# Optimization experiments

Hardware: AMD Instinct MI355X
Metric: run time of the kernel (lower is better)

## Reference

```python
import jax, jax.numpy as jnp
import numpy as np

B, S, D = 2, 2048, 768
HD = 64          # hardcoded head_dim in module
NH = D // HD     # 12 query heads
NKV = max(1, NH // 3)  # 4 kv heads
GROUPS = NH // NKV     # 3
WINDOW = 384
THETA = 10000.0
EPS = 1e-6


def setup_inputs() -> dict:
    key = jax.random.key(0)
    ks = jax.random.split(key, 5)
    return {
        "hidden_states": jax.random.normal(ks[0], (B, S, D), dtype=jnp.float32),
        "q_w": jax.random.normal(ks[1], (NH * HD, D), dtype=jnp.float32) * 0.02,
        "k_w": jax.random.normal(ks[2], (NKV * HD, D), dtype=jnp.float32) * 0.02,
        "v_w": jax.random.normal(ks[3], (NKV * HD, D), dtype=jnp.float32) * 0.02,
        "o_w": jax.random.normal(ks[4], (D, NH * HD), dtype=jnp.float32) * 0.02,
        "q_ln_w": jnp.ones((HD,), dtype=jnp.float32),
        "k_ln_w": jnp.ones((HD,), dtype=jnp.float32),
    }


def _rmsnorm(x, w):
    var = jnp.mean(jnp.square(x.astype(jnp.float32)), axis=-1, keepdims=True)
    return w * (x * jax.lax.rsqrt(var + EPS)).astype(x.dtype)


def _rotate_half(x):
    x1, x2 = jnp.split(x, 2, axis=-1)
    return jnp.concatenate((-x2, x1), axis=-1)


def _rope_cos_sin(seq_len, dtype):
    inv_freq = 1.0 / (THETA ** (jnp.arange(0, HD, 2, dtype=jnp.float32) / HD))
    t = jnp.arange(seq_len, dtype=jnp.float32)
    freqs = jnp.outer(t, inv_freq)            # [S, HD/2]
    emb = jnp.concatenate((freqs, freqs), -1)  # [S, HD]
    return jnp.cos(emb).astype(dtype), jnp.sin(emb).astype(dtype)


def reference(hidden_states, q_w, k_w, v_w, o_w, q_ln_w, k_ln_w):
    b, s, _ = hidden_states.shape
    # projections (nn.Linear: y = x @ W.T)
    q = hidden_states @ q_w.T   # [B,S,NH*HD]
    k = hidden_states @ k_w.T   # [B,S,NKV*HD]
    v = hidden_states @ v_w.T

    q = _rmsnorm(q.reshape(b, s, NH, HD), q_ln_w).transpose(0, 2, 1, 3)      # [B,NH,S,HD]
    k = _rmsnorm(k.reshape(b, s, NKV, HD), k_ln_w).transpose(0, 2, 1, 3)     # [B,NKV,S,HD]
    v = v.reshape(b, s, NKV, HD).transpose(0, 2, 1, 3)                       # [B,NKV,S,HD]

    cos, sin = _rope_cos_sin(s, q.dtype)  # [S,HD]
    cos = cos[None, None]
    sin = sin[None, None]
    q = q * cos + _rotate_half(q) * sin
    k = k * cos + _rotate_half(k) * sin

    # grouped-query repeat: [B,NKV,S,HD] -> [B,NH,S,HD]
    k = jnp.repeat(k, GROUPS, axis=1)
    v = jnp.repeat(v, GROUPS, axis=1)

    scores = jnp.einsum("bhqd,bhkd->bhqk", q, k) / np.sqrt(HD)
    # causal + sliding-window mask: allow i-WINDOW < j <= i
    idx = jnp.arange(s)
    rel = idx[None, :] - idx[:, None]  # j - i
    allowed = (rel <= 0) & (rel > -WINDOW)
    scores = jnp.where(allowed[None, None], scores, -jnp.inf)

    attn = jax.nn.softmax(scores.astype(jnp.float32), axis=-1).astype(q.dtype)
    out = jnp.einsum("bhqk,bhkd->bhqd", attn, v)       # [B,NH,S,HD]
    out = out.transpose(0, 2, 1, 3).reshape(b, s, NH * HD)
    return out @ o_w.T
```

## Files before the change

kernel.cpp:

```cpp
#include <hip/hip_runtime.h>
#include <hip/hip_bf16.h>

typedef __hip_bfloat16 bf16;
typedef __attribute__((ext_vector_type(8))) short bf16x8;
typedef __attribute__((ext_vector_type(4))) float f32x4;

#define MFMA16(a, b, c) __builtin_amdgcn_mfma_f32_16x16x32_bf16((a), (b), (c), 0, 0, 0)


__device__ __forceinline__ void st4bf(bf16* p, float4 v) {
    bf16 t[4];
    t[0] = __float2bfloat16(v.x); t[1] = __float2bfloat16(v.y);
    t[2] = __float2bfloat16(v.z); t[3] = __float2bfloat16(v.w);
    *reinterpret_cast<uint2*>(p) = *reinterpret_cast<const uint2*>(t);
}

__global__ __launch_bounds__(256) void k_prep(
    const float* __restrict__ hs, const float* __restrict__ qw,
    const float* __restrict__ kw, const float* __restrict__ vw,
    const float* __restrict__ ow,
    bf16* __restrict__ hsb, bf16* __restrict__ qwb, bf16* __restrict__ kwb,
    bf16* __restrict__ vwb, bf16* __restrict__ owb, float2* __restrict__ tab)
{
    const int bid = blockIdx.x, tid = threadIdx.x;
    const float* src; bf16* dst; int rel;
    if (bid < 3072)      { src = hs; dst = hsb; rel = bid; }
    else if (bid < 3648) { src = qw; dst = qwb; rel = bid - 3072; }
    else if (bid < 3840) { src = kw; dst = kwb; rel = bid - 3648; }
    else if (bid < 4032) { src = vw; dst = vwb; rel = bid - 3840; }
    else if (bid < 4608) { src = ow; dst = owb; rel = bid - 4032; }
    else {
        int i = (bid - 4608) * 256 + tid;
        int f = i & 31;
        float ang = (float)(i >> 5) * expf(-(float)f * 0.28782313662425572f);
        float sn, cs; sincosf(ang, &sn, &cs);
        tab[i] = make_float2(cs, sn);
        return;
    }
    int i = (rel * 256 + tid) * 4;
    float4 v = *reinterpret_cast<const float4*>(src + i);
    st4bf(dst + i, v);
}

__global__ __launch_bounds__(256) void k_qkv(
    const bf16* __restrict__ hsb, const bf16* __restrict__ qwb,
    const bf16* __restrict__ kwb, const bf16* __restrict__ vwb,
    const float* __restrict__ qln, const float* __restrict__ kln,
    const float2* __restrict__ tab,
    bf16* __restrict__ qo, bf16* __restrict__ ko, bf16* __restrict__ vto)
{
    __shared__ bf16 As[2][64 * 72];
    __shared__ bf16 Bs[2][64 * 72];
    const int tid = threadIdx.x;
    const int w = tid >> 6, l = tid & 63;
    const int lm = l & 15, lg = l >> 4;
    const int m0 = blockIdx.x * 64;
    const int nblk = blockIdx.y;

    const bf16* wsrc; int wrow0, kind, head;
    if (nblk < 12)      { wsrc = qwb; wrow0 = nblk * 64;        kind = 0; head = nblk; }
    else if (nblk < 16) { wsrc = kwb; wrow0 = (nblk - 12) * 64; kind = 1; head = nblk - 12; }
    else                { wsrc = vwb; wrow0 = (nblk - 16) * 64; kind = 2; head = nblk - 16; }

    const int sr = tid >> 2, sc = (tid & 3) * 16;
    const bf16* aptr = hsb  + (size_t)(m0 + sr) * 768 + sc;
    const bf16* bptr = wsrc + (size_t)(wrow0 + sr) * 768 + sc;

    bf16x8 ra0 = *(const bf16x8*)(aptr);
    bf16x8 ra1 = *(const bf16x8*)(aptr + 8);
    bf16x8 rb0 = *(const bf16x8*)(bptr);
    bf16x8 rb1 = *(const bf16x8*)(bptr + 8);
    *(bf16x8*)(&As[0][sr * 72 + sc])     = ra0;
    *(bf16x8*)(&As[0][sr * 72 + sc + 8]) = ra1;
    *(bf16x8*)(&Bs[0][sr * 72 + sc])     = rb0;
    *(bf16x8*)(&Bs[0][sr * 72 + sc + 8]) = rb1;
    __syncthreads();

    f32x4 acc[4] = {};
    for (int t = 0; t < 12; ++t) {
        const int p = t & 1;
        if (t < 11) {
            const bf16* ap = aptr + (t + 1) * 64;
            const bf16* bp = bptr + (t + 1) * 64;
            ra0 = *(const bf16x8*)(ap);
            ra1 = *(const bf16x8*)(ap + 8);
            rb0 = *(const bf16x8*)(bp);
            rb1 = *(const bf16x8*)(bp + 8);
        }
        #pragma unroll
        for (int kk = 0; kk < 2; ++kk) {
            bf16x8 af = *(const bf16x8*)(&As[p][(w * 16 + lm) * 72 + kk * 32 + lg * 8]);
            #pragma unroll
            for (int ct = 0; ct < 4; ++ct) {
                bf16x8 bfr = *(const bf16x8*)(&Bs[p][(ct * 16 + lm) * 72 + kk * 32 + lg * 8]);
                acc[ct] = MFMA16(af, bfr, acc[ct]);
            }
        }
        if (t < 11) {
            __syncthreads();
            *(bf16x8*)(&As[p ^ 1][sr * 72 + sc])     = ra0;
            *(bf16x8*)(&As[p ^ 1][sr * 72 + sc + 8]) = ra1;
            *(bf16x8*)(&Bs[p ^ 1][sr * 72 + sc])     = rb0;
            *(bf16x8*)(&Bs[p ^ 1][sr * 72 + sc + 8]) = rb1;
            __syncthreads();
        }
    }

    const int b  = m0 >> 11;
    const int s0 = m0 & 2047;

    if (kind == 2) {
        bf16* base = vto + (size_t)(b * 4 + head) * 64 * 2048;
        #pragma unroll
        for (int r = 0; r < 4; ++r) {
            const int s = s0 + w * 16 + lg * 4 + r;
            #pragma unroll
            for (int ct = 0; ct < 4; ++ct)
                base[(size_t)(ct * 16 + lm) * 2048 + s] = __float2bfloat16(acc[ct][r]);
        }
        return;
    }

    const float* ln = (kind == 0) ? qln : kln;
    float lw[4];
    #pragma unroll
    for (int ct = 0; ct < 4; ++ct) lw[ct] = ln[ct * 16 + lm];

    bf16* base = (kind == 0) ? qo + ((size_t)(b * 12 + head) * 2048 + s0) * 64
                             : ko + ((size_t)(b * 4  + head) * 2048 + s0) * 64;
    #pragma unroll
    for (int r = 0; r < 4; ++r) {
        float n0 = acc[0][r], n1 = acc[1][r], n2 = acc[2][r], n3 = acc[3][r];
        float ss = n0 * n0 + n1 * n1 + n2 * n2 + n3 * n3;
        ss += __shfl_xor(ss, 1);
        ss += __shfl_xor(ss, 2);
        ss += __shfl_xor(ss, 4);
        ss += __shfl_xor(ss, 8);
        float rms = rsqrtf(ss * (1.0f / 64.0f) + 1e-6f);
        n0 *= rms * lw[0]; n1 *= rms * lw[1]; n2 *= rms * lw[2]; n3 *= rms * lw[3];
        const int row = w * 16 + lg * 4 + r;
        const float2* tp = tab + (size_t)(s0 + row) * 32;
        float2 t0 = tp[lm], t1 = tp[lm + 16];
        bf16* dst = base + (size_t)row * 64;
        dst[lm]      = __float2bfloat16(n0 * t0.x - n2 * t0.y);
        dst[lm + 16] = __float2bfloat16(n1 * t1.x - n3 * t1.y);
        dst[lm + 32] = __float2bfloat16(n2 * t0.x + n0 * t0.y);
        dst[lm + 48] = __float2bfloat16(n3 * t1.x + n1 * t1.y);
    }
}

__global__ __launch_bounds__(256) void k_attn(
    const bf16* __restrict__ qi, const bf16* __restrict__ ki,
    const bf16* __restrict__ vti, bf16* __restrict__ ao)
{
    __shared__ bf16 Ks[2][64 * 72];
    __shared__ bf16 Vs[2][64 * 72];
    __shared__ bf16 Ps[64 * 72];
    const int tid = threadIdx.x;
    const int w = tid >> 6, l = tid & 63;
    const int lm = l & 15, lg = l >> 4;
    const int qb = blockIdx.x, h = blockIdx.y, b = blockIdx.z;
    const int kv = h / 3;
    const int q0 = qb * 64;

    const bf16* qbase = qi + ((size_t)((b * 12 + h) * 2048 + q0 + w * 16 + lm)) * 64 + lg * 8;
    bf16x8 qf0 = *(const bf16x8*)(qbase);
    bf16x8 qf1 = *(const bf16x8*)(qbase + 32);

    f32x4 oacc[4] = {};
    float m_[4], l_[4];
    #pragma unroll
    for (int r = 0; r < 4; ++r) { m_[r] = -INFINITY; l_[r] = 0.f; }

    const int sr = tid >> 2, sc = (tid & 3) * 16;
    const bf16* kgb = ki  + (size_t)(b * 4 + kv) * 2048 * 64;
    const bf16* vgb = vti + (size_t)(b * 4 + kv) * 64 * 2048;

    const int kb_lo = (qb > 6) ? (qb - 6) : 0;
    {
        const bf16* kp = kgb + (size_t)(kb_lo * 64 + sr) * 64 + sc;
        const bf16* vp = vgb + (size_t)sr * 2048 + kb_lo * 64 + sc;
        *(bf16x8*)(&Ks[0][sr * 72 + sc])     = *(const bf16x8*)(kp);
        *(bf16x8*)(&Ks[0][sr * 72 + sc + 8]) = *(const bf16x8*)(kp + 8);
        *(bf16x8*)(&Vs[0][sr * 72 + sc])     = *(const bf16x8*)(vp);
        *(bf16x8*)(&Vs[0][sr * 72 + sc + 8]) = *(const bf16x8*)(vp + 8);
    }
    __syncthreads();

    for (int kb = kb_lo; kb <= qb; ++kb) {
        const int p = (kb - kb_lo) & 1;
        const int k0 = kb * 64;

        bf16x8 rk0, rk1, rv0, rv1;
        if (kb < qb) {
            const bf16* kp = kgb + (size_t)(k0 + 64 + sr) * 64 + sc;
            const bf16* vp = vgb + (size_t)sr * 2048 + k0 + 64 + sc;
            rk0 = *(const bf16x8*)(kp);
            rk1 = *(const bf16x8*)(kp + 8);
            rv0 = *(const bf16x8*)(vp);
            rv1 = *(const bf16x8*)(vp + 8);
        }

        f32x4 sacc[4];
        #pragma unroll
        for (int kt = 0; kt < 4; ++kt) {
            bf16x8 kf0 = *(const bf16x8*)(&Ks[p][(kt * 16 + lm) * 72 + lg * 8]);
            bf16x8 kf1 = *(const bf16x8*)(&Ks[p][(kt * 16 + lm) * 72 + 32 + lg * 8]);
            f32x4 z = {0.f, 0.f, 0.f, 0.f};
            z = MFMA16(qf0, kf0, z);
            sacc[kt] = MFMA16(qf1, kf1, z);
        }

        float pmax[4] = {-INFINITY, -INFINITY, -INFINITY, -INFINITY};
        #pragma unroll
        for (int kt = 0; kt < 4; ++kt)
            #pragma unroll
            for (int r = 0; r < 4; ++r) {
                int kgl = k0 + kt * 16 + lm;
                int qgl = q0 + w * 16 + lg * 4 + r;
                bool ok = (kgl <= qgl) && (kgl > qgl - 384);
                float s = ok ? sacc[kt][r] * 0.125f : -INFINITY;
                sacc[kt][r] = s;
                pmax[r] = fmaxf(pmax[r], s);
            }
        #pragma unroll
        for (int r = 0; r < 4; ++r) {
            float t = pmax[r];
            t = fmaxf(t, __shfl_xor(t, 1));
            t = fmaxf(t, __shfl_xor(t, 2));
            t = fmaxf(t, __shfl_xor(t, 4));
            t = fmaxf(t, __shfl_xor(t, 8));
            pmax[r] = t;
        }

        #pragma unroll
        for (int r = 0; r < 4; ++r) {
            float mnew = fmaxf(m_[r], pmax[r]);
            float scale, rs = 0.f, pv[4];
            if (mnew > -INFINITY) {
                scale = expf(m_[r] - mnew);
                #pragma unroll
                for (int kt = 0; kt < 4; ++kt) { pv[kt] = expf(sacc[kt][r] - mnew); rs += pv[kt]; }
            } else {
                scale = 1.f;
                #pragma unroll
                for (int kt = 0; kt < 4; ++kt) pv[kt] = 0.f;
            }
            m_[r] = mnew;
            rs += __shfl_xor(rs, 1);
            rs += __shfl_xor(rs, 2);
            rs += __shfl_xor(rs, 4);
            rs += __shfl_xor(rs, 8);
            l_[r] = l_[r] * scale + rs;
            #pragma unroll
            for (int dt = 0; dt < 4; ++dt) oacc[dt][r] *= scale;
            #pragma unroll
            for (int kt = 0; kt < 4; ++kt)
                Ps[(w * 16 + lg * 4 + r) * 72 + kt * 16 + lm] = __float2bfloat16(pv[kt]);
        }

        bf16x8 pf0 = *(const bf16x8*)(&Ps[(w * 16 + lm) * 72 + lg * 8]);
        bf16x8 pf1 = *(const bf16x8*)(&Ps[(w * 16 + lm) * 72 + 32 + lg * 8]);
        #pragma unroll
        for (int dt = 0; dt < 4; ++dt) {
            bf16x8 vf0 = *(const bf16x8*)(&Vs[p][(dt * 16 + lm) * 72 + lg * 8]);
            bf16x8 vf1 = *(const bf16x8*)(&Vs[p][(dt * 16 + lm) * 72 + 32 + lg * 8]);
            oacc[dt] = MFMA16(pf0, vf0, oacc[dt]);
            oacc[dt] = MFMA16(pf1, vf1, oacc[dt]);
        }

        if (kb < qb) {
            __syncthreads();
            *(bf16x8*)(&Ks[p ^ 1][sr * 72 + sc])     = rk0;
            *(bf16x8*)(&Ks[p ^ 1][sr * 72 + sc + 8]) = rk1;
            *(bf16x8*)(&Vs[p ^ 1][sr * 72 + sc])     = rv0;
            *(bf16x8*)(&Vs[p ^ 1][sr * 72 + sc + 8]) = rv1;
            __syncthreads();
        }
    }

    #pragma unroll
    for (int r = 0; r < 4; ++r) {
        float inv = 1.f / l_[r];
        bf16* dst = ao + ((size_t)(b * 2048 + q0 + w * 16 + lg * 4 + r)) * 768 + h * 64;
        #pragma unroll
        for (int dt = 0; dt < 4; ++dt)
            dst[dt * 16 + lm] = __float2bfloat16(oacc[dt][r] * inv);
    }
}

__global__ __launch_bounds__(256) void k_oproj(
    const bf16* __restrict__ A, const bf16* __restrict__ W, float* __restrict__ out)
{
    __shared__ bf16 As[2][64 * 72];
    __shared__ bf16 Bs[2][64 * 72];
    const int tid = threadIdx.x;
    const int w = tid >> 6, l = tid & 63;
    const int lm = l & 15, lg = l >> 4;
    const int m0 = blockIdx.x * 64, n0 = blockIdx.y * 64;

    const int sr = tid >> 2, sc = (tid & 3) * 16;
    const bf16* aptr = A + (size_t)(m0 + sr) * 768 + sc;
    const bf16* bptr = W + (size_t)(n0 + sr) * 768 + sc;

    bf16x8 ra0 = *(const bf16x8*)(aptr);
    bf16x8 ra1 = *(const bf16x8*)(aptr + 8);
    bf16x8 rb0 = *(const bf16x8*)(bptr);
    bf16x8 rb1 = *(const bf16x8*)(bptr + 8);
    *(bf16x8*)(&As[0][sr * 72 + sc])     = ra0;
    *(bf16x8*)(&As[0][sr * 72 + sc + 8]) = ra1;
    *(bf16x8*)(&Bs[0][sr * 72 + sc])     = rb0;
    *(bf16x8*)(&Bs[0][sr * 72 + sc + 8]) = rb1;
    __syncthreads();

    f32x4 acc[4] = {};
    for (int t = 0; t < 12; ++t) {
        const int p = t & 1;
        if (t < 11) {
            const bf16* ap = aptr + (t + 1) * 64;
            const bf16* bp = bptr + (t + 1) * 64;
            ra0 = *(const bf16x8*)(ap);
            ra1 = *(const bf16x8*)(ap + 8);
            rb0 = *(const bf16x8*)(bp);
            rb1 = *(const bf16x8*)(bp + 8);
        }
        #pragma unroll
        for (int kk = 0; kk < 2; ++kk) {
            bf16x8 af = *(const bf16x8*)(&As[p][(w * 16 + lm) * 72 + kk * 32 + lg * 8]);
            #pragma unroll
            for (int ct = 0; ct < 4; ++ct) {
                bf16x8 bfr = *(const bf16x8*)(&Bs[p][(ct * 16 + lm) * 72 + kk * 32 + lg * 8]);
                acc[ct] = MFMA16(af, bfr, acc[ct]);
            }
        }
        if (t < 11) {
            __syncthreads();
            *(bf16x8*)(&As[p ^ 1][sr * 72 + sc])     = ra0;
            *(bf16x8*)(&As[p ^ 1][sr * 72 + sc + 8]) = ra1;
            *(bf16x8*)(&Bs[p ^ 1][sr * 72 + sc])     = rb0;
            *(bf16x8*)(&Bs[p ^ 1][sr * 72 + sc + 8]) = rb1;
            __syncthreads();
        }
    }

    #pragma unroll
    for (int r = 0; r < 4; ++r) {
        float* dst = out + (size_t)(m0 + w * 16 + lg * 4 + r) * 768 + n0;
        #pragma unroll
        for (int ct = 0; ct < 4; ++ct)
            dst[ct * 16 + lm] = acc[ct][r];
    }
}

extern "C" void kernel_launch(void* const* d_in, const int* in_sizes, int n_in,
                              void* d_out, int out_size, void* d_ws, size_t ws_size,
                              hipStream_t stream) {
    const float* hs  = (const float*)d_in[0];
    const float* qw  = (const float*)d_in[1];
    const float* kw  = (const float*)d_in[2];
    const float* vw  = (const float*)d_in[3];
    const float* ow  = (const float*)d_in[4];
    const float* qln = (const float*)d_in[5];
    const float* kln = (const float*)d_in[6];
    float* out = (float*)d_out;

    float2* tab  = (float2*)d_ws;
    bf16*   q_ws = (bf16*)(tab + 65536);
    bf16*   k_ws = q_ws + 3145728;
    bf16*   vt_ws= k_ws + 1048576;
    bf16*   x_ws = vt_ws + 1048576;
    bf16*   qwb  = x_ws + 3145728;
    bf16*   kwb  = qwb + 589824;
    bf16*   vwb  = kwb + 196608;
    bf16*   owb  = vwb + 196608;

    k_prep<<<dim3(4864), 256, 0, stream>>>(hs, qw, kw, vw, ow, x_ws, qwb, kwb, vwb, owb, tab);
    k_qkv<<<dim3(64, 20, 1), 256, 0, stream>>>(x_ws, qwb, kwb, vwb, qln, kln, tab, q_ws, k_ws, vt_ws);
    k_attn<<<dim3(32, 12, 2), 256, 0, stream>>>(q_ws, k_ws, vt_ws, x_ws);
    k_oproj<<<dim3(64, 12, 1), 256, 0, stream>>>(x_ws, owb, out);
}
```

Baseline: 73.75 us.

## Use 128x128 block tiles in QKV and output GEMMs; exp2 softmax

Both projection GEMMs move from 64x64 tiles with one 16-row strip per wave to 128x128 tiles, where each wave computes a 64x64 sub-tile from 4x4 MFMA fragments. This gives more operand reuse per LDS fragment load and halves redundant global loads. The trade-off is fewer blocks (320 and 192) on a large GPU, plus more registers and LDS per block. Separately, the attention softmax folds log2(e) into the score scale and uses exp2f instead of expf.

```diff
diff --git a/kernel.cpp b/kernel.cpp
--- a/kernel.cpp
+++ b/kernel.cpp
@@ -49,59 +49,70 @@
     const float2* __restrict__ tab,
     bf16* __restrict__ qo, bf16* __restrict__ ko, bf16* __restrict__ vto)
 {
-    __shared__ bf16 As[2][64 * 72];
-    __shared__ bf16 Bs[2][64 * 72];
+    __shared__ bf16 As[2][128 * 72];
+    __shared__ bf16 Bs[2][128 * 72];
     const int tid = threadIdx.x;
     const int w = tid >> 6, l = tid & 63;
     const int lm = l & 15, lg = l >> 4;
-    const int m0 = blockIdx.x * 64;
+    const int wr = w >> 1, wc = w & 1;
+    const int m0 = blockIdx.x * 128;
     const int nblk = blockIdx.y;
 
-    const bf16* wsrc; int wrow0, kind, head;
-    if (nblk < 12)      { wsrc = qwb; wrow0 = nblk * 64;        kind = 0; head = nblk; }
-    else if (nblk < 16) { wsrc = kwb; wrow0 = (nblk - 12) * 64; kind = 1; head = nblk - 12; }
-    else                { wsrc = vwb; wrow0 = (nblk - 16) * 64; kind = 2; head = nblk - 16; }
-
-    const int sr = tid >> 2, sc = (tid & 3) * 16;
-    const bf16* aptr = hsb  + (size_t)(m0 + sr) * 768 + sc;
-    const bf16* bptr = wsrc + (size_t)(wrow0 + sr) * 768 + sc;
-
-    bf16x8 ra0 = *(const bf16x8*)(aptr);
-    bf16x8 ra1 = *(const bf16x8*)(aptr + 8);
-    bf16x8 rb0 = *(const bf16x8*)(bptr);
-    bf16x8 rb1 = *(const bf16x8*)(bptr + 8);
-    *(bf16x8*)(&As[0][sr * 72 + sc])     = ra0;
-    *(bf16x8*)(&As[0][sr * 72 + sc + 8]) = ra1;
-    *(bf16x8*)(&Bs[0][sr * 72 + sc])     = rb0;
-    *(bf16x8*)(&Bs[0][sr * 72 + sc + 8]) = rb1;
+    const bf16* wsrc; int kind, head;
+    if (nblk < 6)      { wsrc = qwb + (size_t)nblk * 128 * 768;       kind = 0; head = nblk * 2 + wc; }
+    else if (nblk < 8) { wsrc = kwb + (size_t)(nblk - 6) * 128 * 768; kind = 1; head = (nblk - 6) * 2 + wc; }
+    else               { wsrc = vwb + (size_t)(nblk - 8) * 128 * 768; kind = 2; head = (nblk - 8) * 2 + wc; }
+
+    const int sr = tid >> 1, scb = (tid & 1) * 8;
+    const bf16* aptr = hsb  + (size_t)(m0 + sr) * 768 + scb;
+    const bf16* bptr = wsrc + (size_t)sr * 768 + scb;
+
+    bf16x8 ra[4], rb[4];
+    #pragma unroll
+    for (int j = 0; j < 4; ++j) {
+        ra[j] = *(const bf16x8*)(aptr + j * 16);
+        rb[j] = *(const bf16x8*)(bptr + j * 16);
+    }
+    #pragma unroll
+    for (int j = 0; j < 4; ++j) {
+        *(bf16x8*)(&As[0][sr * 72 + scb + j * 16]) = ra[j];
+        *(bf16x8*)(&Bs[0][sr * 72 + scb + j * 16]) = rb[j];
+    }
     __syncthreads();
 
-    f32x4 acc[4] = {};
+    f32x4 acc[4][4] = {};
     for (int t = 0; t < 12; ++t) {
         const int p = t & 1;
         if (t < 11) {
-            const bf16* ap = aptr + (t + 1) * 64;
-            const bf16* bp = bptr + (t + 1) * 64;
-            ra0 = *(const bf16x8*)(ap);
-            ra1 = *(const bf16x8*)(ap + 8);
-            rb0 = *(const bf16x8*)(bp);
-            rb1 = *(const bf16x8*)(bp + 8);
+            const int off = (t + 1) * 64;
+            #pragma unroll
+            for (int j = 0; j < 4; ++j) {
+                ra[j] = *(const bf16x8*)(aptr + off + j * 16);
+                rb[j] = *(const bf16x8*)(bptr + off + j * 16);
+            }
         }
         #pragma unroll
         for (int kk = 0; kk < 2; ++kk) {
-            bf16x8 af = *(const bf16x8*)(&As[p][(w * 16 + lm) * 72 + kk * 32 + lg * 8]);
-            #pragma unroll
-            for (int ct = 0; ct < 4; ++ct) {
-                bf16x8 bfr = *(const bf16x8*)(&Bs[p][(ct * 16 + lm) * 72 + kk * 32 + lg * 8]);
-                acc[ct] = MFMA16(af, bfr, acc[ct]);
-            }
+            bf16x8 af[4], bfv[4];
+            #pragma unroll
+            for (int mf = 0; mf < 4; ++mf)
+                af[mf] = *(const bf16x8*)(&As[p][(wr * 64 + mf * 16 + lm) * 72 + kk * 32 + lg * 8]);
+            #pragma unroll
+            for (int ct = 0; ct < 4; ++ct)
+                bfv[ct] = *(const bf16x8*)(&Bs[p][(wc * 64 + ct * 16 + lm) * 72 + kk * 32 + lg * 8]);
+            #pragma unroll
+            for (int mf = 0; mf < 4; ++mf)
+                #pragma unroll
+                for (int ct = 0; ct < 4; ++ct)
+                    acc[mf][ct] = MFMA16(af[mf], bfv[ct], acc[mf][ct]);
         }
         if (t < 11) {
             __syncthreads();
-            *(bf16x8*)(&As[p ^ 1][sr * 72 + sc])     = ra0;
-            *(bf16x8*)(&As[p ^ 1][sr * 72 + sc + 8]) = ra1;
-            *(bf16x8*)(&Bs[p ^ 1][sr * 72 + sc])     = rb0;
-            *(bf16x8*)(&Bs[p ^ 1][sr * 72 + sc + 8]) = rb1;
+            #pragma unroll
+            for (int j = 0; j < 4; ++j) {
+                *(bf16x8*)(&As[p ^ 1][sr * 72 + scb + j * 16]) = ra[j];
+                *(bf16x8*)(&Bs[p ^ 1][sr * 72 + scb + j * 16]) = rb[j];
+            }
             __syncthreads();
         }
     }
@@ -112,12 +123,14 @@
     if (kind == 2) {
         bf16* base = vto + (size_t)(b * 4 + head) * 64 * 2048;
         #pragma unroll
-        for (int r = 0; r < 4; ++r) {
-            const int s = s0 + w * 16 + lg * 4 + r;
-            #pragma unroll
-            for (int ct = 0; ct < 4; ++ct)
-                base[(size_t)(ct * 16 + lm) * 2048 + s] = __float2bfloat16(acc[ct][r]);
-        }
+        for (int mf = 0; mf < 4; ++mf)
+            #pragma unroll
+            for (int r = 0; r < 4; ++r) {
+                const int s = s0 + wr * 64 + mf * 16 + lg * 4 + r;
+                #pragma unroll
+                for (int ct = 0; ct < 4; ++ct)
+                    base[(size_t)(ct * 16 + lm) * 2048 + s] = __float2bfloat16(acc[mf][ct][r]);
+            }
         return;
     }
 
@@ -129,24 +142,26 @@
     bf16* base = (kind == 0) ? qo + ((size_t)(b * 12 + head) * 2048 + s0) * 64
                              : ko + ((size_t)(b * 4  + head) * 2048 + s0) * 64;
     #pragma unroll
-    for (int r = 0; r < 4; ++r) {
-        float n0 = acc[0][r], n1 = acc[1][r], n2 = acc[2][r], n3 = acc[3][r];
-        float ss = n0 * n0 + n1 * n1 + n2 * n2 + n3 * n3;
-        ss += __shfl_xor(ss, 1);
-        ss += __shfl_xor(ss, 2);
-        ss += __shfl_xor(ss, 4);
-        ss += __shfl_xor(ss, 8);
-        float rms = rsqrtf(ss * (1.0f / 64.0f) + 1e-6f);
-        n0 *= rms * lw[0]; n1 *= rms * lw[1]; n2 *= rms * lw[2]; n3 *= rms * lw[3];
-        const int row = w * 16 + lg * 4 + r;
-        const float2* tp = tab + (size_t)(s0 + row) * 32;
-        float2 t0 = tp[lm], t1 = tp[lm + 16];
-        bf16* dst = base + (size_t)row * 64;
-        dst[lm]      = __float2bfloat16(n0 * t0.x - n2 * t0.y);
-        dst[lm + 16] = __float2bfloat16(n1 * t1.x - n3 * t1.y);
-        dst[lm + 32] = __float2bfloat16(n2 * t0.x + n0 * t0.y);
-        dst[lm + 48] = __float2bfloat16(n3 * t1.x + n1 * t1.y);
-    }
+    for (int mf = 0; mf < 4; ++mf)
+        #pragma unroll
+        for (int r = 0; r < 4; ++r) {
+            float n0 = acc[mf][0][r], n1 = acc[mf][1][r], n2 = acc[mf][2][r], n3 = acc[mf][3][r];
+            float ss = n0 * n0 + n1 * n1 + n2 * n2 + n3 * n3;
+            ss += __shfl_xor(ss, 1);
+            ss += __shfl_xor(ss, 2);
+            ss += __shfl_xor(ss, 4);
+            ss += __shfl_xor(ss, 8);
+            float rms = rsqrtf(ss * (1.0f / 64.0f) + 1e-6f);
+            n0 *= rms * lw[0]; n1 *= rms * lw[1]; n2 *= rms * lw[2]; n3 *= rms * lw[3];
+            const int row = wr * 64 + mf * 16 + lg * 4 + r;
+            const float2* tp = tab + (size_t)(s0 + row) * 32;
+            float2 t0 = tp[lm], t1 = tp[lm + 16];
+            bf16* dst = base + (size_t)row * 64;
+            dst[lm]      = __float2bfloat16(n0 * t0.x - n2 * t0.y);
+            dst[lm + 16] = __float2bfloat16(n1 * t1.x - n3 * t1.y);
+            dst[lm + 32] = __float2bfloat16(n2 * t0.x + n0 * t0.y);
+            dst[lm + 48] = __float2bfloat16(n3 * t1.x + n1 * t1.y);
+        }
 }
 
 __global__ __launch_bounds__(256) void k_attn(
@@ -162,6 +177,7 @@
     const int qb = blockIdx.x, h = blockIdx.y, b = blockIdx.z;
     const int kv = h / 3;
     const int q0 = qb * 64;
+    const float SCL2 = 0.18033688011117042f;
 
     const bf16* qbase = qi + ((size_t)((b * 12 + h) * 2048 + q0 + w * 16 + lm)) * 64 + lg * 8;
     bf16x8 qf0 = *(const bf16x8*)(qbase);
@@ -219,7 +235,7 @@
                 int kgl = k0 + kt * 16 + lm;
                 int qgl = q0 + w * 16 + lg * 4 + r;
                 bool ok = (kgl <= qgl) && (kgl > qgl - 384);
-                float s = ok ? sacc[kt][r] * 0.125f : -INFINITY;
+                float s = ok ? sacc[kt][r] * SCL2 : -INFINITY;
                 sacc[kt][r] = s;
                 pmax[r] = fmaxf(pmax[r], s);
             }
@@ -238,9 +254,9 @@
             float mnew = fmaxf(m_[r], pmax[r]);
             float scale, rs = 0.f, pv[4];
             if (mnew > -INFINITY) {
-                scale = expf(m_[r] - mnew);
+                scale = exp2f(m_[r] - mnew);
                 #pragma unroll
-                for (int kt = 0; kt < 4; ++kt) { pv[kt] = expf(sacc[kt][r] - mnew); rs += pv[kt]; }
+                for (int kt = 0; kt < 4; ++kt) { pv[kt] = exp2f(sacc[kt][r] - mnew); rs += pv[kt]; }
             } else {
                 scale = 1.f;
                 #pragma unroll
@@ -292,64 +308,77 @@
 __global__ __launch_bounds__(256) void k_oproj(
     const bf16* __restrict__ A, const bf16* __restrict__ W, float* __restrict__ out)
 {
-    __shared__ bf16 As[2][64 * 72];
-    __shared__ bf16 Bs[2][64 * 72];
+    __shared__ bf16 As[2][128 * 72];
+    __shared__ bf16 Bs[2][128 * 72];
     const int tid = threadIdx.x;
     const int w = tid >> 6, l = tid & 63;
     const int lm = l & 15, lg = l >> 4;
-    const int m0 = blockIdx.x * 64, n0 = blockIdx.y * 64;
-
-    const int sr = tid >> 2, sc = (tid & 3) * 16;
-    const bf16* aptr = A + (size_t)(m0 + sr) * 768 + sc;
-    const bf16* bptr = W + (size_t)(n0 + sr) * 768 + sc;
-
-    bf16x8 ra0 = *(const bf16x8*)(aptr);
-    bf16x8 ra1 = *(const bf16x8*)(aptr + 8);
-    bf16x8 rb0 = *(const bf16x8*)(bptr);
-    bf16x8 rb1 = *(const bf16x8*)(bptr + 8);
-    *(bf16x8*)(&As[0][sr * 72 + sc])     = ra0;
-    *(bf16x8*)(&As[0][sr * 72 + sc + 8]) = ra1;
-    *(bf16x8*)(&Bs[0][sr * 72 + sc])     = rb0;
-    *(bf16x8*)(&Bs[0][sr * 72 + sc + 8]) = rb1;
+    const int wr = w >> 1, wc = w & 1;
+    const int m0 = blockIdx.x * 128, n0 = blockIdx.y * 128;
+
+    const int sr = tid >> 1, scb = (tid & 1) * 8;
+    const bf16* aptr = A + (size_t)(m0 + sr) * 768 + scb;
+    const bf16* bptr = W + (size_t)(n0 + sr) * 768 + scb;
+
+    bf16x8 ra[4], rb[4];
+    #pragma unroll
+    for (int j = 0; j < 4; ++j) {
+        ra[j] = *(const bf16x8*)(aptr + j * 16);
+        rb[j] = *(const bf16x8*)(bptr + j * 16);
+    }
+    #pragma unroll
+    for (int j = 0; j < 4; ++j) {
+        *(bf16x8*)(&As[0][sr * 72 + scb + j * 16]) = ra[j];
+        *(bf16x8*)(&Bs[0][sr * 72 + scb + j * 16]) = rb[j];
+    }
     __syncthreads();
 
-    f32x4 acc[4] = {};
+    f32x4 acc[4][4] = {};
     for (int t = 0; t < 12; ++t) {
         const int p = t & 1;
         if (t < 11) {
-            const bf16* ap = aptr + (t + 1) * 64;
-            const bf16* bp = bptr + (t + 1) * 64;
-            ra0 = *(const bf16x8*)(ap);
-            ra1 = *(const bf16x8*)(ap + 8);
-            rb0 = *(const bf16x8*)(bp);
-            rb1 = *(const bf16x8*)(bp + 8);
+            const int off = (t + 1) * 64;
+            #pragma unroll
+            for (int j = 0; j < 4; ++j) {
+                ra[j] = *(const bf16x8*)(aptr + off + j * 16);
+                rb[j] = *(const bf16x8*)(bptr + off + j * 16);
+            }
         }
         #pragma unroll
         for (int kk = 0; kk < 2; ++kk) {
-            bf16x8 af = *(const bf16x8*)(&As[p][(w * 16 + lm) * 72 + kk * 32 + lg * 8]);
-            #pragma unroll
-            for (int ct = 0; ct < 4; ++ct) {
-                bf16x8 bfr = *(const bf16x8*)(&Bs[p][(ct * 16 + lm) * 72 + kk * 32 + lg * 8]);
-                acc[ct] = MFMA16(af, bfr, acc[ct]);
-            }
+            bf16x8 af[4], bfv[4];
+            #pragma unroll
+            for (int mf = 0; mf < 4; ++mf)
+                af[mf] = *(const bf16x8*)(&As[p][(wr * 64 + mf * 16 + lm) * 72 + kk * 32 + lg * 8]);
+            #pragma unroll
+            for (int ct = 0; ct < 4; ++ct)
+                bfv[ct] = *(const bf16x8*)(&Bs[p][(wc * 64 + ct * 16 + lm) * 72 + kk * 32 + lg * 8]);
+            #pragma unroll
+            for (int mf = 0; mf < 4; ++mf)
+                #pragma unroll
+                for (int ct = 0; ct < 4; ++ct)
+                    acc[mf][ct] = MFMA16(af[mf], bfv[ct], acc[mf][ct]);
         }
         if (t < 11) {
             __syncthreads();
-            *(bf16x8*)(&As[p ^ 1][sr * 72 + sc])     = ra0;
-            *(bf16x8*)(&As[p ^ 1][sr * 72 + sc + 8]) = ra1;
-            *(bf16x8*)(&Bs[p ^ 1][sr * 72 + sc])     = rb0;
-            *(bf16x8*)(&Bs[p ^ 1][sr * 72 + sc + 8]) = rb1;
-            __syncthreads();
-        }
-    }
-
-    #pragma unroll
-    for (int r = 0; r < 4; ++r) {
-        float* dst = out + (size_t)(m0 + w * 16 + lg * 4 + r) * 768 + n0;
-        #pragma unroll
-        for (int ct = 0; ct < 4; ++ct)
-            dst[ct * 16 + lm] = acc[ct][r];
-    }
+            #pragma unroll
+            for (int j = 0; j < 4; ++j) {
+                *(bf16x8*)(&As[p ^ 1][sr * 72 + scb + j * 16]) = ra[j];
+                *(bf16x8*)(&Bs[p ^ 1][sr * 72 + scb + j * 16]) = rb[j];
+            }
+            __syncthreads();
+        }
+    }
+
+    #pragma unroll
+    for (int mf = 0; mf < 4; ++mf)
+        #pragma unroll
+        for (int r = 0; r < 4; ++r) {
+            float* dst = out + (size_t)(m0 + wr * 64 + mf * 16 + lg * 4 + r) * 768 + n0 + wc * 64;
+            #pragma unroll
+            for (int ct = 0; ct < 4; ++ct)
+                dst[ct * 16 + lm] = acc[mf][ct][r];
+        }
 }
 
 extern "C" void kernel_launch(void* const* d_in, const int* in_sizes, int n_in,
@@ -375,7 +404,7 @@
     bf16*   owb  = vwb + 196608;
 
     k_prep<<<dim3(4864), 256, 0, stream>>>(hs, qw, kw, vw, ow, x_ws, qwb, kwb, vwb, owb, tab);
-    k_qkv<<<dim3(64, 20, 1), 256, 0, stream>>>(x_ws, qwb, kwb, vwb, qln, kln, tab, q_ws, k_ws, vt_ws);
+    k_qkv<<<dim3(32, 10, 1), 256, 0, stream>>>(x_ws, qwb, kwb, vwb, qln, kln, tab, q_ws, k_ws, vt_ws);
     k_attn<<<dim3(32, 12, 2), 256, 0, stream>>>(q_ws, k_ws, vt_ws, x_ws);
-    k_oproj<<<dim3(64, 12, 1), 256, 0, stream>>>(x_ws, owb, out);
-}
+    k_oproj<<<dim3(32, 6, 1), 256, 0, stream>>>(x_ws, owb, out);
+}
```

Result: no change. 74.70 us (+1.3%).

## Use single barrier per tile, exp2 softmax, and skip masking on interior attention tiles

Applied to the files above, without the earlier changes.

The double-buffered LDS pipelines in the QKV projection, attention and output-projection kernels are restructured so each iteration writes the prefetched registers into the current buffer and then needs only one barrier, instead of two barriers around a write to the next buffer. The attention softmax folds log2(e) into the score scale and switches expf to exp2f. Causal/window masking and the -inf guard run only on the diagonal and window-edge key blocks; interior blocks take an unmasked path. This removes barrier and ALU overhead, but correctness of the single-barrier scheme rests on the double buffer keeping a write from overlapping reads of the same buffer.

```diff
diff --git a/kernel.cpp b/kernel.cpp
--- a/kernel.cpp
+++ b/kernel.cpp
@@ -70,22 +70,21 @@
     bf16x8 ra1 = *(const bf16x8*)(aptr + 8);
     bf16x8 rb0 = *(const bf16x8*)(bptr);
     bf16x8 rb1 = *(const bf16x8*)(bptr + 8);
-    *(bf16x8*)(&As[0][sr * 72 + sc])     = ra0;
-    *(bf16x8*)(&As[0][sr * 72 + sc + 8]) = ra1;
-    *(bf16x8*)(&Bs[0][sr * 72 + sc])     = rb0;
-    *(bf16x8*)(&Bs[0][sr * 72 + sc + 8]) = rb1;
-    __syncthreads();
 
     f32x4 acc[4] = {};
     for (int t = 0; t < 12; ++t) {
         const int p = t & 1;
+        *(bf16x8*)(&As[p][sr * 72 + sc])     = ra0;
+        *(bf16x8*)(&As[p][sr * 72 + sc + 8]) = ra1;
+        *(bf16x8*)(&Bs[p][sr * 72 + sc])     = rb0;
+        *(bf16x8*)(&Bs[p][sr * 72 + sc + 8]) = rb1;
+        __syncthreads();
         if (t < 11) {
-            const bf16* ap = aptr + (t + 1) * 64;
-            const bf16* bp = bptr + (t + 1) * 64;
-            ra0 = *(const bf16x8*)(ap);
-            ra1 = *(const bf16x8*)(ap + 8);
-            rb0 = *(const bf16x8*)(bp);
-            rb1 = *(const bf16x8*)(bp + 8);
+            const int off = (t + 1) * 64;
+            ra0 = *(const bf16x8*)(aptr + off);
+            ra1 = *(const bf16x8*)(aptr + off + 8);
+            rb0 = *(const bf16x8*)(bptr + off);
+            rb1 = *(const bf16x8*)(bptr + off + 8);
         }
         #pragma unroll
         for (int kk = 0; kk < 2; ++kk) {
@@ -95,14 +94,6 @@
                 bf16x8 bfr = *(const bf16x8*)(&Bs[p][(ct * 16 + lm) * 72 + kk * 32 + lg * 8]);
                 acc[ct] = MFMA16(af, bfr, acc[ct]);
             }
-        }
-        if (t < 11) {
-            __syncthreads();
-            *(bf16x8*)(&As[p ^ 1][sr * 72 + sc])     = ra0;
-            *(bf16x8*)(&As[p ^ 1][sr * 72 + sc + 8]) = ra1;
-            *(bf16x8*)(&Bs[p ^ 1][sr * 72 + sc])     = rb0;
-            *(bf16x8*)(&Bs[p ^ 1][sr * 72 + sc + 8]) = rb1;
-            __syncthreads();
         }
     }
 
@@ -162,6 +153,7 @@
     const int qb = blockIdx.x, h = blockIdx.y, b = blockIdx.z;
     const int kv = h / 3;
     const int q0 = qb * 64;
+    const float SCL2 = 0.18033688011117042f;
 
     const bf16* qbase = qi + ((size_t)((b * 12 + h) * 2048 + q0 + w * 16 + lm)) * 64 + lg * 8;
     bf16x8 qf0 = *(const bf16x8*)(qbase);
@@ -177,21 +169,25 @@
     const bf16* vgb = vti + (size_t)(b * 4 + kv) * 64 * 2048;
 
     const int kb_lo = (qb > 6) ? (qb - 6) : 0;
+    bf16x8 rk0, rk1, rv0, rv1;
     {
         const bf16* kp = kgb + (size_t)(kb_lo * 64 + sr) * 64 + sc;
         const bf16* vp = vgb + (size_t)sr * 2048 + kb_lo * 64 + sc;
-        *(bf16x8*)(&Ks[0][sr * 72 + sc])     = *(const bf16x8*)(kp);
-        *(bf16x8*)(&Ks[0][sr * 72 + sc + 8]) = *(const bf16x8*)(kp + 8);
-        *(bf16x8*)(&Vs[0][sr * 72 + sc])     = *(const bf16x8*)(vp);
-        *(bf16x8*)(&Vs[0][sr * 72 + sc + 8]) = *(const bf16x8*)(vp + 8);
-    }
-    __syncthreads();
+        rk0 = *(const bf16x8*)(kp);
+        rk1 = *(const bf16x8*)(kp + 8);
+        rv0 = *(const bf16x8*)(vp);
+        rv1 = *(const bf16x8*)(vp + 8);
+    }
 
     for (int kb = kb_lo; kb <= qb; ++kb) {
         const int p = (kb - kb_lo) & 1;
         const int k0 = kb * 64;
 
-        bf16x8 rk0, rk1, rv0, rv1;
+        *(bf16x8*)(&Ks[p][sr * 72 + sc])     = rk0;
+        *(bf16x8*)(&Ks[p][sr * 72 + sc + 8]) = rk1;
+        *(bf16x8*)(&Vs[p][sr * 72 + sc])     = rv0;
+        *(bf16x8*)(&Vs[p][sr * 72 + sc + 8]) = rv1;
+        __syncthreads();
         if (kb < qb) {
             const bf16* kp = kgb + (size_t)(k0 + 64 + sr) * 64 + sc;
             const bf16* vp = vgb + (size_t)sr * 2048 + k0 + 64 + sc;
@@ -212,17 +208,29 @@
         }
 
         float pmax[4] = {-INFINITY, -INFINITY, -INFINITY, -INFINITY};
-        #pragma unroll
-        for (int kt = 0; kt < 4; ++kt)
-            #pragma unroll
-            for (int r = 0; r < 4; ++r) {
-                int kgl = k0 + kt * 16 + lm;
-                int qgl = q0 + w * 16 + lg * 4 + r;
-                bool ok = (kgl <= qgl) && (kgl > qgl - 384);
-                float s = ok ? sacc[kt][r] * 0.125f : -INFINITY;
-                sacc[kt][r] = s;
-                pmax[r] = fmaxf(pmax[r], s);
-            }
+        const bool need_mask = (kb == qb) || (kb == qb - 6);
+        if (need_mask) {
+            #pragma unroll
+            for (int kt = 0; kt < 4; ++kt)
+                #pragma unroll
+                for (int r = 0; r < 4; ++r) {
+                    int kgl = k0 + kt * 16 + lm;
+                    int qgl = q0 + w * 16 + lg * 4 + r;
+                    bool ok = (kgl <= qgl) && (kgl > qgl - 384);
+                    float s = ok ? sacc[kt][r] * SCL2 : -INFINITY;
+                    sacc[kt][r] = s;
+                    pmax[r] = fmaxf(pmax[r], s);
+                }
+        } else {
+            #pragma unroll
+            for (int kt = 0; kt < 4; ++kt)
+                #pragma unroll
+                for (int r = 0; r < 4; ++r) {
+                    float s = sacc[kt][r] * SCL2;
+                    sacc[kt][r] = s;
+                    pmax[r] = fmaxf(pmax[r], s);
+                }
+        }
         #pragma unroll
         for (int r = 0; r < 4; ++r) {
             float t = pmax[r];
@@ -233,30 +241,52 @@
             pmax[r] = t;
         }
 
-        #pragma unroll
-        for (int r = 0; r < 4; ++r) {
-            float mnew = fmaxf(m_[r], pmax[r]);
-            float scale, rs = 0.f, pv[4];
-            if (mnew > -INFINITY) {
-                scale = expf(m_[r] - mnew);
-                #pragma unroll
-                for (int kt = 0; kt < 4; ++kt) { pv[kt] = expf(sacc[kt][r] - mnew); rs += pv[kt]; }
-            } else {
-                scale = 1.f;
-                #pragma unroll
-                for (int kt = 0; kt < 4; ++kt) pv[kt] = 0.f;
+        if (need_mask) {
+            #pragma unroll
+            for (int r = 0; r < 4; ++r) {
+                float mnew = fmaxf(m_[r], pmax[r]);
+                float scale, rs = 0.f, pv[4];
+                if (mnew > -INFINITY) {
+                    scale = exp2f(m_[r] - mnew);
+                    #pragma unroll
+                    for (int kt = 0; kt < 4; ++kt) { pv[kt] = exp2f(sacc[kt][r] - mnew); rs += pv[kt]; }
+                } else {
+                    scale = 1.f;
+                    #pragma unroll
+                    for (int kt = 0; kt < 4; ++kt) pv[kt] = 0.f;
+                }
+                m_[r] = mnew;
+                rs += __shfl_xor(rs, 1);
+                rs += __shfl_xor(rs, 2);
+                rs += __shfl_xor(rs, 4);
+                rs += __shfl_xor(rs, 8);
+                l_[r] = l_[r] * scale + rs;
+                #pragma unroll
+                for (int dt = 0; dt < 4; ++dt) oacc[dt][r] *= scale;
+                #pragma unroll
+                for (int kt = 0; kt < 4; ++kt)
+                    Ps[(w * 16 + lg * 4 + r) * 72 + kt * 16 + lm] = __float2bfloat16(pv[kt]);
             }
-            m_[r] = mnew;
-            rs += __shfl_xor(rs, 1);
-            rs += __shfl_xor(rs, 2);
-            rs += __shfl_xor(rs, 4);
-            rs += __shfl_xor(rs, 8);
-            l_[r] = l_[r] * scale + rs;
-            #pragma unroll
-            for (int dt = 0; dt < 4; ++dt) oacc[dt][r] *= scale;
-            #pragma unroll
-            for (int kt = 0; kt < 4; ++kt)
-                Ps[(w * 16 + lg * 4 + r) * 72 + kt * 16 + lm] = __float2bfloat16(pv[kt]);
+        } else {
+            #pragma unroll
+            for (int r = 0; r < 4; ++r) {
+                float mnew = fmaxf(m_[r], pmax[r]);
+                float scale = exp2f(m_[r] - mnew);
+                float rs = 0.f, pv[4];
+                #pragma unroll
+                for (int kt = 0; kt < 4; ++kt) { pv[kt] = exp2f(sacc[kt][r] - mnew); rs += pv[kt]; }
+                m_[r] = mnew;
+                rs += __shfl_xor(rs, 1);
+                rs += __shfl_xor(rs, 2);
+                rs += __shfl_xor(rs, 4);
+                rs += __shfl_xor(rs, 8);
+                l_[r] = l_[r] * scale + rs;
+                #pragma unroll
+                for (int dt = 0; dt < 4; ++dt) oacc[dt][r] *= scale;
+                #pragma unroll
+                for (int kt = 0; kt < 4; ++kt)
+                    Ps[(w * 16 + lg * 4 + r) * 72 + kt * 16 + lm] = __float2bfloat16(pv[kt]);
+            }
         }
 
         bf16x8 pf0 = *(const bf16x8*)(&Ps[(w * 16 + lm) * 72 + lg * 8]);
@@ -267,15 +297,6 @@
             bf16x8 vf1 = *(const bf16x8*)(&Vs[p][(dt * 16 + lm) * 72 + 32 + lg * 8]);
             oacc[dt] = MFMA16(pf0, vf0, oacc[dt]);
             oacc[dt] = MFMA16(pf1, vf1, oacc[dt]);
-        }
-
-        if (kb < qb) {
-            __syncthreads();
-            *(bf16x8*)(&Ks[p ^ 1][sr * 72 + sc])     = rk0;
-            *(bf16x8*)(&Ks[p ^ 1][sr * 72 + sc + 8]) = rk1;
-            *(bf16x8*)(&Vs[p ^ 1][sr * 72 + sc])     = rv0;
-            *(bf16x8*)(&Vs[p ^ 1][sr * 72 + sc + 8]) = rv1;
-            __syncthreads();
         }
     }
 
@@ -307,22 +328,21 @@
     bf16x8 ra1 = *(const bf16x8*)(aptr + 8);
     bf16x8 rb0 = *(const bf16x8*)(bptr);
     bf16x8 rb1 = *(const bf16x8*)(bptr + 8);
-    *(bf16x8*)(&As[0][sr * 72 + sc])     = ra0;
-    *(bf16x8*)(&As[0][sr * 72 + sc + 8]) = ra1;
-    *(bf16x8*)(&Bs[0][sr * 72 + sc])     = rb0;
-    *(bf16x8*)(&Bs[0][sr * 72 + sc + 8]) = rb1;
-    __syncthreads();
 
     f32x4 acc[4] = {};
     for (int t = 0; t < 12; ++t) {
         const int p = t & 1;
+        *(bf16x8*)(&As[p][sr * 72 + sc])     = ra0;
+        *(bf16x8*)(&As[p][sr * 72 + sc + 8]) = ra1;
+        *(bf16x8*)(&Bs[p][sr * 72 + sc])     = rb0;
+        *(bf16x8*)(&Bs[p][sr * 72 + sc + 8]) = rb1;
+        __syncthreads();
         if (t < 11) {
-            const bf16* ap = aptr + (t + 1) * 64;
-            const bf16* bp = bptr + (t + 1) * 64;
-            ra0 = *(const bf16x8*)(ap);
-            ra1 = *(const bf16x8*)(ap + 8);
-            rb0 = *(const bf16x8*)(bp);
-            rb1 = *(const bf16x8*)(bp + 8);
+            const int off = (t + 1) * 64;
+            ra0 = *(const bf16x8*)(aptr + off);
+            ra1 = *(const bf16x8*)(aptr + off + 8);
+            rb0 = *(const bf16x8*)(bptr + off);
+            rb1 = *(const bf16x8*)(bptr + off + 8);
         }
         #pragma unroll
         for (int kk = 0; kk < 2; ++kk) {
@@ -332,14 +352,6 @@
                 bf16x8 bfr = *(const bf16x8*)(&Bs[p][(ct * 16 + lm) * 72 + kk * 32 + lg * 8]);
                 acc[ct] = MFMA16(af, bfr, acc[ct]);
             }
-        }
-        if (t < 11) {
-            __syncthreads();
-            *(bf16x8*)(&As[p ^ 1][sr * 72 + sc])     = ra0;
-            *(bf16x8*)(&As[p ^ 1][sr * 72 + sc + 8]) = ra1;
-            *(bf16x8*)(&Bs[p ^ 1][sr * 72 + sc])     = rb0;
-            *(bf16x8*)(&Bs[p ^ 1][sr * 72 + sc + 8]) = rb1;
-            __syncthreads();
         }
     }
 
```

New measurement: 69.49 us. -5.8%, faster.
